# Kernel tuning notes

Hardware: AMD Instinct MI355X
Metric: run time of the kernel (lower is better)

The kernel has to match this reference:

```python
import jax, jax.numpy as jnp
import numpy as np

NUM_MESHES = 8
NUM_FACES = 16384
NUM_NEIGHBOR = 3
SAMPLES_PER_NEIGHBOR = 8
NUM_SAMPLES = NUM_NEIGHBOR * SAMPLES_PER_NEIGHBOR  # 24
NUM_KERNEL = 64


def setup_inputs() -> dict:
    key = jax.random.key(0)
    ks = jax.random.split(key, 8)
    centers = jax.random.normal(ks[0], (NUM_MESHES, NUM_FACES, 3), dtype=jnp.float32)
    ring_n = jax.random.randint(ks[1], (NUM_MESHES, NUM_FACES, NUM_NEIGHBOR), 0, NUM_FACES)
    neighbor_corners = jax.random.normal(ks[2], (NUM_MESHES, NUM_FACES, NUM_NEIGHBOR, 3, 3), dtype=jnp.float32)
    # AlphaBetaGamma.initialize(): barycentric weights from r1, r2
    r1 = jax.random.uniform(ks[3], (NUM_FACES, NUM_SAMPLES), dtype=jnp.float32)
    r2 = jax.random.uniform(ks[4], (NUM_FACES, NUM_SAMPLES), dtype=jnp.float32)
    r1_sqrt = jnp.sqrt(r1)
    alpha = 1.0 - r1_sqrt
    beta = r1_sqrt * (1.0 - r2)
    gamma = r1_sqrt * r2
    W = jax.random.normal(ks[5], (NUM_KERNEL, 3), dtype=jnp.float32) * 0.1
    b = jnp.zeros((NUM_KERNEL,), dtype=jnp.float32)
    return {"centers": centers, "ring_n": ring_n, "neighbor_corners": neighbor_corners,
            "alpha": alpha, "beta": beta, "gamma": gamma, "W": W, "b": b}


def reference(centers, ring_n, neighbor_corners, alpha, beta, gamma, W, b):
    # Uniform neighbor resampling: tile each neighbor SAMPLES_PER_NEIGHBOR times
    # (torch.cat([neighbor_corners] * freq, dim=2))
    rs_nc = jnp.concatenate([neighbor_corners] * SAMPLES_PER_NEIGHBOR, axis=2)  # [M,F,S,3,3]
    c1, c2, c3 = rs_nc[:, :, :, 0, :], rs_nc[:, :, :, 1, :], rs_nc[:, :, :, 2, :]
    # barycentric surface points on neighbor faces: [M,F,S,3]
    a = alpha[None, :, :, None]
    bt = beta[None, :, :, None]
    g = gamma[None, :, :, None]
    points = a * c1 + bt * c2 + g * c3
    # geodesic direction vectors from face center to surface points
    dirs = points - centers[:, :, None, :]  # [M,F,S,3]
    # per-point kernel response, ReLU, then max over samples
    fea = jax.nn.relu(jnp.einsum('mfsc,kc->mfsk', dirs, W) + b)  # [M,F,S,K]
    out = jnp.max(fea, axis=2)  # [M,F,K]
    return out
```

## Files before the change

kernel.cpp:

```cpp
#include <hip/hip_runtime.h>


#define NM 8
#define NF 16384
#define NK 64

#define NEI(MX, T, S0,S1,S2,S3,S4,S5,S6,S7) do { \
    const float a1_ = T[0]*w0 + T[1]*w1 + T[2]*w2; \
    const float a2_ = T[3]*w0 + T[4]*w1 + T[5]*w2; \
    const float a3_ = T[6]*w0 + T[7]*w1 + T[8]*w2; \
    const float e2_ = a2_ - a1_, e3_ = a3_ - a1_; \
    const float v0_ = fmaf(bs##S0, e2_, fmaf(gs##S0, e3_, a1_)); \
    const float v1_ = fmaf(bs##S1, e2_, fmaf(gs##S1, e3_, a1_)); \
    const float v2_ = fmaf(bs##S2, e2_, fmaf(gs##S2, e3_, a1_)); \
    const float v3_ = fmaf(bs##S3, e2_, fmaf(gs##S3, e3_, a1_)); \
    const float v4_ = fmaf(bs##S4, e2_, fmaf(gs##S4, e3_, a1_)); \
    const float v5_ = fmaf(bs##S5, e2_, fmaf(gs##S5, e3_, a1_)); \
    const float v6_ = fmaf(bs##S6, e2_, fmaf(gs##S6, e3_, a1_)); \
    const float v7_ = fmaf(bs##S7, e2_, fmaf(gs##S7, e3_, a1_)); \
    const float p0_ = fmaxf(fmaxf(v0_, v1_), v2_); \
    const float p1_ = fmaxf(fmaxf(v3_, v4_), v5_); \
    const float p2_ = fmaxf(fmaxf(v6_, v7_), p0_); \
    MX = fmaxf(MX, fmaxf(p1_, p2_)); \
} while (0)

__global__ __launch_bounds__(256, 8) void conv_surface_kernel(
    const float* __restrict__ centers,
    const float* __restrict__ nc,
    const float* __restrict__ beta,
    const float* __restrict__ gammav,
    const float* __restrict__ W,
    const float* __restrict__ b,
    float* __restrict__ out)
{
    const int tid  = threadIdx.x;
    const int lane = tid & 63;
    const int fdiv = blockIdx.x * 4 + (tid >> 6);
    const int funi = __builtin_amdgcn_readfirstlane(fdiv);

    const float w0 = W[lane * 3 + 0];
    const float w1 = W[lane * 3 + 1];
    const float w2 = W[lane * 3 + 2];
    const float bk = b[lane];

    const float* __restrict__ bpp = beta   + (size_t)funi * 24;
    const float* __restrict__ gpp = gammav + (size_t)funi * 24;
    const float bs0 =bpp[0],  bs1 =bpp[1],  bs2 =bpp[2],  bs3 =bpp[3];
    const float bs4 =bpp[4],  bs5 =bpp[5],  bs6 =bpp[6],  bs7 =bpp[7];
    const float bs8 =bpp[8],  bs9 =bpp[9],  bs10=bpp[10], bs11=bpp[11];
    const float bs12=bpp[12], bs13=bpp[13], bs14=bpp[14], bs15=bpp[15];
    const float bs16=bpp[16], bs17=bpp[17], bs18=bpp[18], bs19=bpp[19];
    const float bs20=bpp[20], bs21=bpp[21], bs22=bpp[22], bs23=bpp[23];
    const float gs0 =gpp[0],  gs1 =gpp[1],  gs2 =gpp[2],  gs3 =gpp[3];
    const float gs4 =gpp[4],  gs5 =gpp[5],  gs6 =gpp[6],  gs7 =gpp[7];
    const float gs8 =gpp[8],  gs9 =gpp[9],  gs10=gpp[10], gs11=gpp[11];
    const float gs12=gpp[12], gs13=gpp[13], gs14=gpp[14], gs15=gpp[15];
    const float gs16=gpp[16], gs17=gpp[17], gs18=gpp[18], gs19=gpp[19];
    const float gs20=gpp[20], gs21=gpp[21], gs22=gpp[22], gs23=gpp[23];

    const float* __restrict__ tb = nc      + (size_t)fdiv * 27;
    const float* __restrict__ cb = centers + (size_t)fdiv * 3;
    float* __restrict__       ob = out     + (size_t)fdiv * NK + lane;

#pragma unroll
    for (int m = 0; m < NM; ++m) {
        const float* __restrict__ t = tb + (size_t)m * (NF * 27);
        const float* __restrict__ c = cb + (size_t)m * (NF * 3);

        const float cdot = c[0] * w0 + c[1] * w1 + c[2] * w2;

        float mx = -3.4e38f;
        NEI(mx, (t + 0), 0, 3, 6, 9, 12, 15, 18, 21);
        NEI(mx, (t + 9), 1, 4, 7, 10, 13, 16, 19, 22);
        NEI(mx, (t + 18), 2, 5, 8, 11, 14, 17, 20, 23);

        ob[(size_t)m * (NF * NK)] = fmaxf(mx + (bk - cdot), 0.0f);
    }
}

extern "C" void kernel_launch(void* const* d_in, const int* in_sizes, int n_in,
                              void* d_out, int out_size, void* d_ws, size_t ws_size,
                              hipStream_t stream) {
    const float* centers = (const float*)d_in[0];
    const float* nc      = (const float*)d_in[2];
    const float* beta    = (const float*)d_in[4];
    const float* gammav  = (const float*)d_in[5];
    const float* W       = (const float*)d_in[6];
    const float* b       = (const float*)d_in[7];
    float* out = (float*)d_out;

    dim3 grid(NF / 4), block(256);
    hipLaunchKernelGGL(conv_surface_kernel, grid, block, 0, stream,
                       centers, nc, beta, gammav, W, b, out);
}
```

Before: 38.92 us.

## Load per-face data with one coalesced vector load and broadcast via readlane

Before this, every lane loaded the same uniform beta/gamma, corner and center values, which the compiler likely turned into scalar loads. Now each lane loads one element, so the 48 beta/gamma values and the 27 corner plus 3 center values per mesh come in as a single vector load each. The values are then broadcast to all lanes with readlane. All eight mesh loads are issued up front, and the launch bound drops to 4 waves per SIMD so more registers are available. The cost is many readlane instructions and lower occupancy.

```diff
diff --git a/kernel.cpp b/kernel.cpp
--- a/kernel.cpp
+++ b/kernel.cpp
@@ -5,10 +5,15 @@
 #define NF 16384
 #define NK 64
 
-#define NEI(MX, T, S0,S1,S2,S3,S4,S5,S6,S7) do { \
-    const float a1_ = T[0]*w0 + T[1]*w1 + T[2]*w2; \
-    const float a2_ = T[3]*w0 + T[4]*w1 + T[5]*w2; \
-    const float a3_ = T[6]*w0 + T[7]*w1 + T[8]*w2; \
+#define RL(V, I) __int_as_float(__builtin_amdgcn_readlane(__float_as_int(V), (I)))
+
+#define NEI(MX, DM, E, S0,S1,S2,S3,S4,S5,S6,S7) do { \
+    const float t0_ = RL(DM, (E)+0), t1_ = RL(DM, (E)+1), t2_ = RL(DM, (E)+2); \
+    const float t3_ = RL(DM, (E)+3), t4_ = RL(DM, (E)+4), t5_ = RL(DM, (E)+5); \
+    const float t6_ = RL(DM, (E)+6), t7_ = RL(DM, (E)+7), t8_ = RL(DM, (E)+8); \
+    const float a1_ = t0_*w0 + t1_*w1 + t2_*w2; \
+    const float a2_ = t3_*w0 + t4_*w1 + t5_*w2; \
+    const float a3_ = t6_*w0 + t7_*w1 + t8_*w2; \
     const float e2_ = a2_ - a1_, e3_ = a3_ - a1_; \
     const float v0_ = fmaf(bs##S0, e2_, fmaf(gs##S0, e3_, a1_)); \
     const float v1_ = fmaf(bs##S1, e2_, fmaf(gs##S1, e3_, a1_)); \
@@ -24,7 +29,17 @@
     MX = fmaxf(MX, fmaxf(p1_, p2_)); \
 } while (0)
 
-__global__ __launch_bounds__(256, 8) void conv_surface_kernel(
+#define MESH(M, DM) do { \
+    const float cx_ = RL(DM, 27), cy_ = RL(DM, 28), cz_ = RL(DM, 29); \
+    const float cdot_ = cx_*w0 + cy_*w1 + cz_*w2; \
+    float mx_ = -3.4e38f; \
+    NEI(mx_, DM, 0,  0,3,6,9,12,15,18,21); \
+    NEI(mx_, DM, 9,  1,4,7,10,13,16,19,22); \
+    NEI(mx_, DM, 18, 2,5,8,11,14,17,20,23); \
+    out[((size_t)(M) * NF + funi) * NK + lane] = fmaxf(mx_ + (bk - cdot_), 0.0f); \
+} while (0)
+
+__global__ __launch_bounds__(256, 4) void conv_surface_kernel(
     const float* __restrict__ centers,
     const float* __restrict__ nc,
     const float* __restrict__ beta,
@@ -35,47 +50,52 @@
 {
     const int tid  = threadIdx.x;
     const int lane = tid & 63;
-    const int fdiv = blockIdx.x * 4 + (tid >> 6);
-    const int funi = __builtin_amdgcn_readfirstlane(fdiv);
+    const int funi = __builtin_amdgcn_readfirstlane(blockIdx.x * 4 + (tid >> 6));
 
     const float w0 = W[lane * 3 + 0];
     const float w1 = W[lane * 3 + 1];
     const float w2 = W[lane * 3 + 2];
     const float bk = b[lane];
 
-    const float* __restrict__ bpp = beta   + (size_t)funi * 24;
-    const float* __restrict__ gpp = gammav + (size_t)funi * 24;
-    const float bs0 =bpp[0],  bs1 =bpp[1],  bs2 =bpp[2],  bs3 =bpp[3];
-    const float bs4 =bpp[4],  bs5 =bpp[5],  bs6 =bpp[6],  bs7 =bpp[7];
-    const float bs8 =bpp[8],  bs9 =bpp[9],  bs10=bpp[10], bs11=bpp[11];
-    const float bs12=bpp[12], bs13=bpp[13], bs14=bpp[14], bs15=bpp[15];
-    const float bs16=bpp[16], bs17=bpp[17], bs18=bpp[18], bs19=bpp[19];
-    const float bs20=bpp[20], bs21=bpp[21], bs22=bpp[22], bs23=bpp[23];
-    const float gs0 =gpp[0],  gs1 =gpp[1],  gs2 =gpp[2],  gs3 =gpp[3];
-    const float gs4 =gpp[4],  gs5 =gpp[5],  gs6 =gpp[6],  gs7 =gpp[7];
-    const float gs8 =gpp[8],  gs9 =gpp[9],  gs10=gpp[10], gs11=gpp[11];
-    const float gs12=gpp[12], gs13=gpp[13], gs14=gpp[14], gs15=gpp[15];
-    const float gs16=gpp[16], gs17=gpp[17], gs18=gpp[18], gs19=gpp[19];
-    const float gs20=gpp[20], gs21=gpp[21], gs22=gpp[22], gs23=gpp[23];
+    const int lb = (lane < 48) ? lane : 0;
+    const float bgv = (lb < 24)
+        ? beta  [(size_t)funi * 24 + lb]
+        : gammav[(size_t)funi * 24 + (lb - 24)];
+    const float bs0 =RL(bgv, 0), bs1 =RL(bgv, 1), bs2 =RL(bgv, 2), bs3 =RL(bgv, 3);
+    const float bs4 =RL(bgv, 4), bs5 =RL(bgv, 5), bs6 =RL(bgv, 6), bs7 =RL(bgv, 7);
+    const float bs8 =RL(bgv, 8), bs9 =RL(bgv, 9), bs10=RL(bgv,10), bs11=RL(bgv,11);
+    const float bs12=RL(bgv,12), bs13=RL(bgv,13), bs14=RL(bgv,14), bs15=RL(bgv,15);
+    const float bs16=RL(bgv,16), bs17=RL(bgv,17), bs18=RL(bgv,18), bs19=RL(bgv,19);
+    const float bs20=RL(bgv,20), bs21=RL(bgv,21), bs22=RL(bgv,22), bs23=RL(bgv,23);
+    const float gs0 =RL(bgv,24), gs1 =RL(bgv,25), gs2 =RL(bgv,26), gs3 =RL(bgv,27);
+    const float gs4 =RL(bgv,28), gs5 =RL(bgv,29), gs6 =RL(bgv,30), gs7 =RL(bgv,31);
+    const float gs8 =RL(bgv,32), gs9 =RL(bgv,33), gs10=RL(bgv,34), gs11=RL(bgv,35);
+    const float gs12=RL(bgv,36), gs13=RL(bgv,37), gs14=RL(bgv,38), gs15=RL(bgv,39);
+    const float gs16=RL(bgv,40), gs17=RL(bgv,41), gs18=RL(bgv,42), gs19=RL(bgv,43);
+    const float gs20=RL(bgv,44), gs21=RL(bgv,45), gs22=RL(bgv,46), gs23=RL(bgv,47);
 
-    const float* __restrict__ tb = nc      + (size_t)fdiv * 27;
-    const float* __restrict__ cb = centers + (size_t)fdiv * 3;
-    float* __restrict__       ob = out     + (size_t)fdiv * NK + lane;
+    const int ll = (lane < 30) ? lane : 0;
+    const float* __restrict__ ga = (ll < 27)
+        ? (nc      + (size_t)funi * 27 + ll)
+        : (centers + (size_t)funi * 3  + (ll - 27));
+    const size_t st = (ll < 27) ? (size_t)NF * 27 : (size_t)NF * 3;
+    const float d0 = ga[0];
+    const float d1 = ga[st];
+    const float d2 = ga[2 * st];
+    const float d3 = ga[3 * st];
+    const float d4 = ga[4 * st];
+    const float d5 = ga[5 * st];
+    const float d6 = ga[6 * st];
+    const float d7 = ga[7 * st];
 
-#pragma unroll
-    for (int m = 0; m < NM; ++m) {
-        const float* __restrict__ t = tb + (size_t)m * (NF * 27);
-        const float* __restrict__ c = cb + (size_t)m * (NF * 3);
-
-        const float cdot = c[0] * w0 + c[1] * w1 + c[2] * w2;
-
-        float mx = -3.4e38f;
-        NEI(mx, (t + 0), 0, 3, 6, 9, 12, 15, 18, 21);
-        NEI(mx, (t + 9), 1, 4, 7, 10, 13, 16, 19, 22);
-        NEI(mx, (t + 18), 2, 5, 8, 11, 14, 17, 20, 23);
-
-        ob[(size_t)m * (NF * NK)] = fmaxf(mx + (bk - cdot), 0.0f);
-    }
+    MESH(0, d0);
+    MESH(1, d1);
+    MESH(2, d2);
+    MESH(3, d3);
+    MESH(4, d4);
+    MESH(5, d5);
+    MESH(6, d6);
+    MESH(7, d7);
 }
 
 extern "C" void kernel_launch(void* const* d_in, const int* in_sizes, int n_in,
```

Result: slower. 39.75 us (+2.1%).
